# Performance work log

Measured on AMD Instinct MI355X. Metric: run time of the kernel, lower is better.

## Reference

```python
import jax, jax.numpy as jnp
import numpy as np

NUM_SAMPLES = 1024  # from init_kwargs


def _fps(x, num_samples):
    """Iterative farthest-point sampling.

    x: [B, N, C] float point cloud.
    Returns (sampled_points [B, S, C], indices [B, S] int32).
    Starts from point 0 in each cloud (deterministic seed point).
    """
    B, N, C = x.shape
    barange = jnp.arange(B)
    init_idx = jnp.zeros((B,), dtype=jnp.int32)
    init_min = jnp.full((B, N), jnp.inf, dtype=x.dtype)

    def step(carry, _):
        min_d, cur = carry
        pt = x[barange, cur]                                  # [B, C] current farthest point
        d = jnp.sum((x - pt[:, None, :]) ** 2, axis=-1)       # [B, N] squared dist to it
        min_d = jnp.minimum(min_d, d)                         # running min-dist to sampled set
        nxt = jnp.argmax(min_d, axis=1).astype(jnp.int32)     # next farthest point per cloud
        return (min_d, nxt), cur                              # emit the index we just consumed

    (_, _), idxs = jax.lax.scan(step, (init_min, init_idx), None, length=num_samples)
    idxs = jnp.transpose(idxs)                                # [B, S]
    sampled = jnp.take_along_axis(x, idxs[..., None], axis=1)  # [B, S, C]
    return sampled, idxs


def setup_inputs() -> dict:
    key = jax.random.key(0)
    x = jax.random.uniform(key, (64, 32768, 3), dtype=jnp.float32)
    return {"x": x}


def reference(x):
    return _fps(x, NUM_SAMPLES)
```

## Files before the change

kernel.cpp:

```cpp
#include <hip/hip_runtime.h>


#define FPS_N   32768
#define FPS_S   1024
#define FPS_NT  1024
#define FPS_P   32
#define NPAIR   (FPS_P / 2)
#define PAIRS_B (FPS_N / 2)

__global__ __launch_bounds__(256) void fps_repack(
    const float* __restrict__ x, float4* __restrict__ xy4, int B)
{
    const int g = blockIdx.x * 256 + threadIdx.x;
    if (g >= B * PAIRS_B) return;
    const int b  = g / PAIRS_B;
    const int p  = g - b * PAIRS_B;
    const int j2 = p >> 10;
    const int t  = p & 1023;
    const int i0 = j2 * 2048 + t;
    const float* __restrict__ xb = x + (size_t)b * FPS_N * 3;
    float4 v;
    v.x = xb[(size_t)i0 * 3 + 0];
    v.y = xb[(size_t)i0 * 3 + 1];
    v.z = xb[(size_t)(i0 + 1024) * 3 + 0];
    v.w = xb[(size_t)(i0 + 1024) * 3 + 1];
    xy4[(size_t)b * PAIRS_B + p] = v;
}

__global__ __launch_bounds__(FPS_NT, 4) void FPSModel_80753975099708_kernel(
    const float* __restrict__ x,
    const float4* __restrict__ xy4,
    float* __restrict__ out_pts,
    float* __restrict__ out_idx)
{
#pragma clang fp contract(off)
    const int b = blockIdx.x;
    const int t = threadIdx.x;
    const float* __restrict__ xb = x + (size_t)b * FPS_N * 3;
    const float4* __restrict__ xy4b = xy4 + (size_t)b * PAIRS_B;
    float* __restrict__ op = out_pts + (size_t)b * FPS_S * 3;
    float* __restrict__ oi = out_idx + (size_t)b * FPS_S;

    __shared__ float zs[FPS_N];
    __shared__ float2 red[2][FPS_NT / 64];

    float mind[FPS_P];

#pragma unroll
    for (int k = 0; k < FPS_P; ++k) {
        const int i = k * FPS_NT + t;
        zs[i] = xb[(size_t)i * 3 + 2];
        mind[k] = __int_as_float(0x7f800000);
    }

    int cur = 0;
    if (t == 0) {
        oi[0] = 0.0f;
        op[0] = xb[0];
        op[1] = xb[1];
        op[2] = xb[2];
    }
    __syncthreads();

    for (int s = 1; s < FPS_S; ++s) {
        const float px = xb[(size_t)cur * 3 + 0];
        const float py = xb[(size_t)cur * 3 + 1];
        const float pz = xb[(size_t)cur * 3 + 2];

        float bestv = __int_as_float(0xff800000);
        int   besti = 0x7fffffff;

#pragma unroll
        for (int j2 = 0; j2 < NPAIR; ++j2) {
            const float4 v = xy4b[j2 * FPS_NT + t];
            const int ia = j2 * 2048 + t;
            const float za = zs[ia];
            const float zb = zs[ia + 1024];
            {
                const float dx = v.x - px;
                const float dy = v.y - py;
                const float dz = za - pz;
                const float d  = __builtin_fmaf(dz, dz,
                                  __builtin_fmaf(dx, dx, dy * dy));
                const float m = fminf(mind[2 * j2], d);
                mind[2 * j2] = m;
                if (m > bestv) { bestv = m; besti = ia; }
            }
            {
                const float dx = v.z - px;
                const float dy = v.w - py;
                const float dz = zb - pz;
                const float d  = __builtin_fmaf(dz, dz,
                                  __builtin_fmaf(dx, dx, dy * dy));
                const float m = fminf(mind[2 * j2 + 1], d);
                mind[2 * j2 + 1] = m;
                if (m > bestv) { bestv = m; besti = ia + 1024; }
            }
        }

#pragma unroll
        for (int off = 32; off; off >>= 1) {
            const float ov = __shfl_xor(bestv, off);
            const int   ob = __shfl_xor(besti, off);
            if (ov > bestv || (ov == bestv && ob < besti)) { bestv = ov; besti = ob; }
        }

        if ((t & 63) == 0) {
            red[s & 1][t >> 6] = make_float2(bestv, __int_as_float(besti));
        }
        __syncthreads();

        float gv = __int_as_float(0xff800000);
        int   gi = 0x7fffffff;
#pragma unroll
        for (int w = 0; w < FPS_NT / 64; ++w) {
            const float2 e = red[s & 1][w];
            const int ei = __float_as_int(e.y);
            if (e.x > gv || (e.x == gv && ei < gi)) { gv = e.x; gi = ei; }
        }
        cur = gi;

        if (t == 0) {
            oi[s] = (float)cur;
            const float* __restrict__ p = xb + (size_t)cur * 3;
            op[(size_t)s * 3 + 0] = p[0];
            op[(size_t)s * 3 + 1] = p[1];
            op[(size_t)s * 3 + 2] = p[2];
        }
    }
}

extern "C" void kernel_launch(void* const* d_in, const int* in_sizes, int n_in,
                              void* d_out, int out_size, void* d_ws, size_t ws_size,
                              hipStream_t stream) {
    const float* x = (const float*)d_in[0];
    const int B = in_sizes[0] / (FPS_N * 3);

    float* out_pts = (float*)d_out;
    float* out_idx = out_pts + (size_t)B * FPS_S * 3;
    float4* xy4 = (float4*)d_ws;

    const int total = B * PAIRS_B;
    hipLaunchKernelGGL(fps_repack, dim3((total + 255) / 256), dim3(256),
                       0, stream, x, xy4, B);

    hipLaunchKernelGGL(FPSModel_80753975099708_kernel,
                       dim3(B), dim3(FPS_NT), 0, stream,
                       x, xy4, out_pts, out_idx);
}
```

Measured before the change: 3.919 ms.

## Use packed FP32 math, tree argmax reductions and u64 keys in FPS loop

After: 3.819 ms. 1.03x faster.

```diff
diff --git a/kernel.cpp b/kernel.cpp
--- a/kernel.cpp
+++ b/kernel.cpp
@@ -1,11 +1,14 @@
 #include <hip/hip_runtime.h>
 
+
+typedef float f32x2 __attribute__((ext_vector_type(2)));
+typedef unsigned long long u64;
+typedef unsigned int u32;
 
 #define FPS_N   32768
 #define FPS_S   1024
 #define FPS_NT  1024
-#define FPS_P   32
-#define NPAIR   (FPS_P / 2)
+#define NPAIR   16
 #define PAIRS_B (FPS_N / 2)
 
 __global__ __launch_bounds__(256) void fps_repack(
@@ -17,19 +20,21 @@
     const int p  = g - b * PAIRS_B;
     const int j2 = p >> 10;
     const int t  = p & 1023;
-    const int i0 = j2 * 2048 + t;
+    const int ia = j2 * 2048 + t;
     const float* __restrict__ xb = x + (size_t)b * FPS_N * 3;
     float4 v;
-    v.x = xb[(size_t)i0 * 3 + 0];
-    v.y = xb[(size_t)i0 * 3 + 1];
-    v.z = xb[(size_t)(i0 + 1024) * 3 + 0];
-    v.w = xb[(size_t)(i0 + 1024) * 3 + 1];
+    v.x = xb[(size_t)ia * 3 + 0];
+    v.y = xb[(size_t)(ia + 1024) * 3 + 0];
+    v.z = xb[(size_t)ia * 3 + 1];
+    v.w = xb[(size_t)(ia + 1024) * 3 + 1];
     xy4[(size_t)b * PAIRS_B + p] = v;
 }
 
-__global__ __launch_bounds__(FPS_NT, 4) void FPSModel_80753975099708_kernel(
+__global__ __launch_bounds__(FPS_NT)
+__attribute__((amdgpu_waves_per_eu(4, 4)))
+void FPSModel_80753975099708_kernel(
     const float* __restrict__ x,
-    const float4* __restrict__ xy4,
+    const f32x2* __restrict__ xy2,
     float* __restrict__ out_pts,
     float* __restrict__ out_idx)
 {
@@ -37,20 +42,22 @@
     const int b = blockIdx.x;
     const int t = threadIdx.x;
     const float* __restrict__ xb = x + (size_t)b * FPS_N * 3;
-    const float4* __restrict__ xy4b = xy4 + (size_t)b * PAIRS_B;
+    const f32x2* __restrict__ xyb = xy2 + (size_t)b * PAIRS_B * 2;
     float* __restrict__ op = out_pts + (size_t)b * FPS_S * 3;
     float* __restrict__ oi = out_idx + (size_t)b * FPS_S;
 
-    __shared__ float zs[FPS_N];
-    __shared__ float2 red[2][FPS_NT / 64];
+    __shared__ float2 zs2[PAIRS_B];
+    __shared__ u64 red[2][FPS_NT / 64];
 
-    float mind[FPS_P];
+    float mind[2 * NPAIR];
 
 #pragma unroll
-    for (int k = 0; k < FPS_P; ++k) {
-        const int i = k * FPS_NT + t;
-        zs[i] = xb[(size_t)i * 3 + 2];
-        mind[k] = __int_as_float(0x7f800000);
+    for (int j2 = 0; j2 < NPAIR; ++j2) {
+        const int ia = j2 * 2048 + t;
+        zs2[j2 * FPS_NT + t] =
+            make_float2(xb[(size_t)ia * 3 + 2], xb[(size_t)(ia + 1024) * 3 + 2]);
+        mind[2 * j2]     = __int_as_float(0x7f800000);
+        mind[2 * j2 + 1] = __int_as_float(0x7f800000);
     }
 
     int cur = 0;
@@ -63,62 +70,72 @@
     __syncthreads();
 
     for (int s = 1; s < FPS_S; ++s) {
-        const float px = xb[(size_t)cur * 3 + 0];
-        const float py = xb[(size_t)cur * 3 + 1];
-        const float pz = xb[(size_t)cur * 3 + 2];
+        const int curU = __builtin_amdgcn_readfirstlane(cur);
+        const float px = xb[(size_t)curU * 3 + 0];
+        const float py = xb[(size_t)curU * 3 + 1];
+        const float pz = xb[(size_t)curU * 3 + 2];
+        f32x2 NX, NY, NZ;
+        NX[0] = -px; NX[1] = -px;
+        NY[0] = -py; NY[1] = -py;
+        NZ[0] = -pz; NZ[1] = -pz;
 
-        float bestv = __int_as_float(0xff800000);
-        int   besti = 0x7fffffff;
+        float v0[NPAIR];
+        int   k0[NPAIR];
 
 #pragma unroll
         for (int j2 = 0; j2 < NPAIR; ++j2) {
-            const float4 v = xy4b[j2 * FPS_NT + t];
-            const int ia = j2 * 2048 + t;
-            const float za = zs[ia];
-            const float zb = zs[ia + 1024];
-            {
-                const float dx = v.x - px;
-                const float dy = v.y - py;
-                const float dz = za - pz;
-                const float d  = __builtin_fmaf(dz, dz,
-                                  __builtin_fmaf(dx, dx, dy * dy));
-                const float m = fminf(mind[2 * j2], d);
-                mind[2 * j2] = m;
-                if (m > bestv) { bestv = m; besti = ia; }
-            }
-            {
-                const float dx = v.z - px;
-                const float dy = v.w - py;
-                const float dz = zb - pz;
-                const float d  = __builtin_fmaf(dz, dz,
-                                  __builtin_fmaf(dx, dx, dy * dy));
-                const float m = fminf(mind[2 * j2 + 1], d);
-                mind[2 * j2 + 1] = m;
-                if (m > bestv) { bestv = m; besti = ia + 1024; }
-            }
+            const f32x2 X = xyb[2 * (j2 * FPS_NT + t)];
+            const f32x2 Y = xyb[2 * (j2 * FPS_NT + t) + 1];
+            const f32x2 Z = *(const f32x2*)&zs2[j2 * FPS_NT + t];
+            f32x2 DX, DY, DZ, T, T2, D;
+            asm("v_pk_add_f32 %0, %1, %2" : "=v"(DX) : "v"(X), "v"(NX));
+            asm("v_pk_add_f32 %0, %1, %2" : "=v"(DY) : "v"(Y), "v"(NY));
+            asm("v_pk_add_f32 %0, %1, %2" : "=v"(DZ) : "v"(Z), "v"(NZ));
+            asm("v_pk_mul_f32 %0, %1, %1" : "=v"(T)  : "v"(DY));
+            asm("v_pk_fma_f32 %0, %1, %1, %2" : "=v"(T2) : "v"(DX), "v"(T));
+            asm("v_pk_fma_f32 %0, %1, %1, %2" : "=v"(D)  : "v"(DZ), "v"(T2));
+            const float ma = fminf(mind[2 * j2],     D[0]);
+            const float mb = fminf(mind[2 * j2 + 1], D[1]);
+            mind[2 * j2]     = ma;
+            mind[2 * j2 + 1] = mb;
+            const bool g0 = mb > ma;
+            v0[j2] = g0 ? mb : ma;
+            k0[j2] = g0 ? (2 * j2 + 1) : (2 * j2);
         }
 
 #pragma unroll
+        for (int st = 1; st < NPAIR; st <<= 1) {
+#pragma unroll
+            for (int j = 0; j < NPAIR; j += 2 * st) {
+                const bool g2 = v0[j + st] > v0[j];
+                v0[j] = g2 ? v0[j + st] : v0[j];
+                k0[j] = g2 ? k0[j + st] : k0[j];
+            }
+        }
+        const u32 besti = (u32)(k0[0] * FPS_NT + t);
+        u64 key = ((u64)__float_as_uint(v0[0]) << 32) |
+                  (u64)(0xFFFFFFFFu - besti);
+
+#pragma unroll
         for (int off = 32; off; off >>= 1) {
-            const float ov = __shfl_xor(bestv, off);
-            const int   ob = __shfl_xor(besti, off);
-            if (ov > bestv || (ov == bestv && ob < besti)) { bestv = ov; besti = ob; }
+            const u64 ok = __shfl_xor((unsigned long long)key, off);
+            if (ok > key) key = ok;
         }
 
-        if ((t & 63) == 0) {
-            red[s & 1][t >> 6] = make_float2(bestv, __int_as_float(besti));
-        }
+        if ((t & 63) == 0) red[s & 1][t >> 6] = key;
         __syncthreads();
 
-        float gv = __int_as_float(0xff800000);
-        int   gi = 0x7fffffff;
+        u64 r0[FPS_NT / 64];
 #pragma unroll
-        for (int w = 0; w < FPS_NT / 64; ++w) {
-            const float2 e = red[s & 1][w];
-            const int ei = __float_as_int(e.y);
-            if (e.x > gv || (e.x == gv && ei < gi)) { gv = e.x; gi = ei; }
+        for (int w = 0; w < FPS_NT / 64; ++w) r0[w] = red[s & 1][w];
+#pragma unroll
+        for (int st = 1; st < FPS_NT / 64; st <<= 1) {
+#pragma unroll
+            for (int w = 0; w < FPS_NT / 64; w += 2 * st) {
+                if (r0[w + st] > r0[w]) r0[w] = r0[w + st];
+            }
         }
-        cur = gi;
+        cur = (int)(0xFFFFFFFFu - (u32)(r0[0] & 0xFFFFFFFFull));
 
         if (t == 0) {
             oi[s] = (float)cur;
@@ -146,5 +163,5 @@
 
     hipLaunchKernelGGL(FPSModel_80753975099708_kernel,
                        dim3(B), dim3(FPS_NT), 0, stream,
-                       x, xy4, out_pts, out_idx);
+                       x, (const f32x2*)xy4, out_pts, out_idx);
 }
```
